# Kernel optimization log

Measured on AMD Instinct MI355X. Metric: run time of the kernel, lower is better.

Reference implementation:

```python
import jax, jax.numpy as jnp
import numpy as np

B, S, C, H, D = 2, 2048, 1024, 16, 64  # hidden C must equal H*D (value is a reshape of key_states)


def setup_inputs() -> dict:
    key = jax.random.key(0)
    ks = jax.random.split(key, 7)
    query_states = jax.random.normal(ks[0], (B, S, C), dtype=jnp.float32)
    key_states = jax.random.normal(ks[1], (B, S, C), dtype=jnp.float32)
    attention_mask = jax.random.randint(ks[2], (B, 1, 1, S), 0, 2).astype(jnp.int32)
    Wq = jax.random.normal(ks[3], (C, H, D), dtype=jnp.float32) * 0.02
    bq = jnp.zeros((H, D), dtype=jnp.float32)
    Wk = jax.random.normal(ks[4], (C, H, D), dtype=jnp.float32) * 0.02
    bk = jnp.zeros((H, D), dtype=jnp.float32)
    return {
        "query_states": query_states,
        "key_states": key_states,
        "attention_mask": attention_mask,
        "Wq": Wq,
        "bq": bq,
        "Wk": Wk,
        "bk": bk,
    }


def reference(query_states, key_states, attention_mask, Wq, bq, Wk, bk):
    # EinsumDense 'abc,cde->abde' with bias on 'de'
    q = jnp.einsum("bsc,chd->bshd", query_states, Wq) + bq  # [B,S,H,D]
    k = jnp.einsum("bsc,chd->bshd", key_states, Wk) + bk    # [B,S,H,D]
    # value is just key_states reshaped into head layout (no projection!)
    v = key_states.reshape(k.shape)                          # [B,S,H,D]
    # scale query by 1/sqrt(dk)
    q = q * jax.lax.rsqrt(jnp.asarray(D, q.dtype))
    # 'aecd,abcd->acbe': a=batch, c=head, b=query pos, e=key pos
    scores = jnp.einsum("bkhd,bqhd->bhqk", k, q)             # [B,H,Sq,Sk]
    mask = (1.0 - attention_mask.astype(scores.dtype)) * -10000.0
    scores = scores + mask
    probs = jax.nn.softmax(scores, axis=-1)
    # dropout is identity at training=False (default)
    # 'acbe,aecd->abcd': weighted sum of values over key positions
    out = jnp.einsum("bhqk,bkhd->bqhd", probs, v)            # [B,S,H,D]
    return out
```

## Files before the change

kernel.cpp:

```cpp
#include <hip/hip_runtime.h>

#define BSZ 2
#define SEQ 2048
#define CH  1024
#define NH  16
#define HD  64
#define LOG2E 1.4426950408889634f

typedef short  bf16x8 __attribute__((ext_vector_type(8)));
typedef short  bf16x4 __attribute__((ext_vector_type(4)));
typedef float  f32x4  __attribute__((ext_vector_type(4)));

__device__ __forceinline__ short f2bf(float f) {
    union { float f; unsigned u; } v; v.f = f;
    unsigned r = v.u + 0x7FFFu + ((v.u >> 16) & 1u);
    return (short)(r >> 16);
}
__device__ __forceinline__ short f2bf_fast(float f) {
    union { float f; unsigned u; } v; v.f = f;
    return (short)((v.u + 0x8000u) >> 16);
}

#if __has_builtin(__builtin_amdgcn_mfma_f32_16x16x16bf16_1k)
__device__ __forceinline__ f32x4 mfma16x16x16(bf16x4 a, bf16x4 b, f32x4 c) {
    return __builtin_amdgcn_mfma_f32_16x16x16bf16_1k(a, b, c, 0, 0, 0);
}
#else
__device__ __forceinline__ f32x4 mfma16x16x16(bf16x4 a, bf16x4 b, f32x4 c) {
    f32x4 d;
    asm("v_mfma_f32_16x16x16_bf16 %0, %1, %2, %3"
        : "=v"(d) : "v"(a), "v"(b), "v"(c));
    return d;
}
#endif

__global__ __launch_bounds__(256) void cast_bf16(
    const float* __restrict__ a, const float* __restrict__ b,
    short* __restrict__ da, short* __restrict__ db)
{
    const float* s = blockIdx.y ? b : a;
    short*       d = blockIdx.y ? db : da;
    long i = ((long)blockIdx.x * 256 + threadIdx.x) * 8;
    float4 v0 = *(const float4*)&s[i];
    float4 v1 = *(const float4*)&s[i + 4];
    bf16x8 o;
    o[0] = f2bf(v0.x); o[1] = f2bf(v0.y); o[2] = f2bf(v0.z); o[3] = f2bf(v0.w);
    o[4] = f2bf(v1.x); o[5] = f2bf(v1.y); o[6] = f2bf(v1.z); o[7] = f2bf(v1.w);
    *(bf16x8*)&d[i] = o;
}

__global__ __launch_bounds__(256) void transpose_cast(
    const float* __restrict__ src, short* __restrict__ dst,
    long sb0, long sb1, long db0, long db1, int srs, int drs)
{
    __shared__ float tile[64][65];
    const int z = blockIdx.z;
    const float* s = src + (long)(z >> 4) * sb0 + (long)(z & 15) * sb1;
    short*       d = dst + (long)(z >> 4) * db0 + (long)(z & 15) * db1;
    const int r0 = blockIdx.y * 64, c0 = blockIdx.x * 64;
    const int tid = threadIdx.x;
    const int r  = tid >> 2;
    const int c4 = (tid & 3) << 4;

    #pragma unroll
    for (int i = 0; i < 16; i += 4) {
        float4 v = *(const float4*)&s[(long)(r0 + r) * srs + c0 + c4 + i];
        tile[r][c4 + i + 0] = v.x;
        tile[r][c4 + i + 1] = v.y;
        tile[r][c4 + i + 2] = v.z;
        tile[r][c4 + i + 3] = v.w;
    }
    __syncthreads();
    bf16x8 o0, o1;
    #pragma unroll
    for (int i = 0; i < 8; i++) o0[i] = f2bf(tile[c4 + i][r]);
    #pragma unroll
    for (int i = 0; i < 8; i++) o1[i] = f2bf(tile[c4 + 8 + i][r]);
    *(bf16x8*)&d[(long)(c0 + r) * drs + r0 + c4 + 0] = o0;
    *(bf16x8*)&d[(long)(c0 + r) * drs + r0 + c4 + 8] = o1;
}

__global__ __launch_bounds__(256) void mask_prep(
    const int* __restrict__ am, float* __restrict__ mf)
{
    int i = blockIdx.x * 256 + threadIdx.x;
    mf[i] = (1.0f - (float)am[i]) * (-10000.0f * LOG2E);
}

__global__ __launch_bounds__(256, 2) void proj_mfma(
    const short* __restrict__ Xq, const short* __restrict__ Xk,
    const short* __restrict__ Wtq, const short* __restrict__ Wtk,
    const float* __restrict__ bq_, const float* __restrict__ bk_,
    short* __restrict__ Yq, short* __restrict__ Yk)
{
    __shared__ short At[128 * 72];
    __shared__ short Bt[128 * 72];
    const int zz = blockIdx.z;
    const short* X    = zz ? Xk  : Xq;
    const short* Wt   = zz ? Wtk : Wtq;
    const float* bias = zz ? bk_ : bq_;
    short*       Y    = zz ? Yk  : Yq;
    const float scale = zz ? 1.0f : (0.125f * LOG2E);

    const int tid  = threadIdx.x;
    const int lane = tid & 63, w = tid >> 6;
    const int quad = lane >> 4, t16 = lane & 15;
    const int m0 = blockIdx.y * 128, n0 = blockIdx.x * 128;
    const int srow = tid >> 1;
    const int shalf = (tid & 1) * 32;

    f32x4 acc[4][4];
    #pragma unroll
    for (int i = 0; i < 4; i++)
        #pragma unroll
        for (int j = 0; j < 4; j++)
            acc[i][j] = (f32x4){0.f, 0.f, 0.f, 0.f};

    const int M0 = (w >> 1) * 64, N0 = (w & 1) * 64;

    bf16x8 ar[4], br[4];
    #pragma unroll
    for (int c = 0; c < 4; c++) {
        ar[c] = *(const bf16x8*)&X [(long)(m0 + srow) * CH + shalf + 8 * c];
        br[c] = *(const bf16x8*)&Wt[(long)(n0 + srow) * CH + shalf + 8 * c];
    }

    for (int k0 = 0; k0 < CH; k0 += 64) {
        __syncthreads();
        #pragma unroll
        for (int c = 0; c < 4; c++) {
            *(bf16x8*)&At[srow * 72 + shalf + 8 * c] = ar[c];
            *(bf16x8*)&Bt[srow * 72 + shalf + 8 * c] = br[c];
        }
        __syncthreads();

        if (k0 + 64 < CH) {
            #pragma unroll
            for (int c = 0; c < 4; c++) {
                ar[c] = *(const bf16x8*)&X [(long)(m0 + srow) * CH + k0 + 64 + shalf + 8 * c];
                br[c] = *(const bf16x8*)&Wt[(long)(n0 + srow) * CH + k0 + 64 + shalf + 8 * c];
            }
        }

        #pragma unroll
        for (int kk = 0; kk < 2; kk++) {
            bf16x8 af[4], bw[4];
            #pragma unroll
            for (int im = 0; im < 4; im++)
                af[im] = *(bf16x8*)&At[(M0 + 16 * im + t16) * 72 + kk * 32 + quad * 8];
            #pragma unroll
            for (int jn = 0; jn < 4; jn++)
                bw[jn] = *(bf16x8*)&Bt[(N0 + 16 * jn + t16) * 72 + kk * 32 + quad * 8];
            #pragma unroll
            for (int im = 0; im < 4; im++)
                #pragma unroll
                for (int jn = 0; jn < 4; jn++)
                    acc[im][jn] = __builtin_amdgcn_mfma_f32_16x16x32_bf16(
                        af[im], bw[jn], acc[im][jn], 0, 0, 0);
        }
    }

    #pragma unroll
    for (int jn = 0; jn < 4; jn++) {
        float bs = bias[n0 + N0 + 16 * jn + t16];
        #pragma unroll
        for (int im = 0; im < 4; im++)
            #pragma unroll
            for (int reg = 0; reg < 4; reg++) {
                float y = (acc[im][jn][reg] + bs) * scale;
                Y[(long)(m0 + M0 + 16 * im + 4 * quad + reg) * (NH * HD)
                  + n0 + N0 + 16 * jn + t16] = f2bf(y);
            }
    }
}

__global__ __launch_bounds__(256, 2) void attn_mfma(
    const short* __restrict__ qp,
    const short* __restrict__ kp,
    const short* __restrict__ vt,
    const float* __restrict__ mf,
    float* __restrict__ out)
{
    __shared__ short Kt[64 * 72];
    __shared__ short Vt[64 * 72];

    const int qt0 = blockIdx.x * 128;
    const int h   = blockIdx.y;
    const int b   = blockIdx.z;
    const int tid = threadIdx.x;
    const int lane = tid & 63, w = tid >> 6;
    const int quad = lane >> 4, t16 = lane & 15;

    bf16x8 qf[2][2];
    #pragma unroll
    for (int qm = 0; qm < 2; qm++)
        #pragma unroll
        for (int ds = 0; ds < 2; ds++)
            qf[qm][ds] = *(const bf16x8*)&qp[
                (long)(b * SEQ + qt0 + w * 32 + qm * 16 + t16) * CH
                + h * HD + ds * 32 + quad * 8];

    f32x4 oa[4][2];
    float l_r[2];
    #pragma unroll
    for (int dt = 0; dt < 4; dt++)
        #pragma unroll
        for (int qm = 0; qm < 2; qm++)
            oa[dt][qm] = (f32x4){0.f, 0.f, 0.f, 0.f};
    l_r[0] = l_r[1] = 0.f;

    const int srow  = tid >> 2;
    const int scol  = (tid & 3) * 16;
    const long kbase = (long)(b * SEQ) * CH + h * HD;
    const long vbase = ((long)(b * NH + h) * HD) * SEQ;

    bf16x8 kr[2], vr[2];
    #pragma unroll
    for (int c = 0; c < 2; c++) {
        kr[c] = *(const bf16x8*)&kp[kbase + (long)srow * CH + scol + 8 * c];
        vr[c] = *(const bf16x8*)&vt[vbase + (long)srow * SEQ + scol + 8 * c];
    }

    for (int kt0 = 0; kt0 < SEQ; kt0 += 64) {
        __syncthreads();
        #pragma unroll
        for (int c = 0; c < 2; c++) {
            *(bf16x8*)&Kt[srow * 72 + scol + 8 * c] = kr[c];
            *(bf16x8*)&Vt[srow * 72 + scol + 8 * c] = vr[c];
        }
        __syncthreads();

        if (kt0 + 64 < SEQ) {
            #pragma unroll
            for (int c = 0; c < 2; c++) {
                kr[c] = *(const bf16x8*)&kp[kbase + (long)(kt0 + 64 + srow) * CH + scol + 8 * c];
                vr[c] = *(const bf16x8*)&vt[vbase + (long)srow * SEQ + kt0 + 64 + scol + 8 * c];
            }
        }

        float4 mv4[4];
        #pragma unroll
        for (int jt = 0; jt < 4; jt++)
            mv4[jt] = *(const float4*)&mf[b * SEQ + kt0 + jt * 16 + quad * 4];

        f32x4 sa[2][4];
        #pragma unroll
        for (int qm = 0; qm < 2; qm++)
            #pragma unroll
            for (int jt = 0; jt < 4; jt++) sa[qm][jt] = (f32x4){0.f, 0.f, 0.f, 0.f};
        #pragma unroll
        for (int ds = 0; ds < 2; ds++) {
            bf16x8 kb[4];
            #pragma unroll
            for (int jt = 0; jt < 4; jt++)
                kb[jt] = *(bf16x8*)&Kt[(jt * 16 + t16) * 72 + ds * 32 + quad * 8];
            #pragma unroll
            for (int qm = 0; qm < 2; qm++)
                #pragma unroll
                for (int jt = 0; jt < 4; jt++)
                    sa[qm][jt] = __builtin_amdgcn_mfma_f32_16x16x32_bf16(
                        kb[jt], qf[qm][ds], sa[qm][jt], 0, 0, 0);
        }

        bf16x4 pb[2][4];
        #pragma unroll
        for (int qm = 0; qm < 2; qm++)
            #pragma unroll
            for (int jt = 0; jt < 4; jt++) {
                float p0 = exp2f(sa[qm][jt][0] + mv4[jt].x);
                float p1 = exp2f(sa[qm][jt][1] + mv4[jt].y);
                float p2 = exp2f(sa[qm][jt][2] + mv4[jt].z);
                float p3 = exp2f(sa[qm][jt][3] + mv4[jt].w);
                l_r[qm] += (p0 + p1) + (p2 + p3);
                bf16x4 pk;
                pk[0] = f2bf_fast(p0); pk[1] = f2bf_fast(p1);
                pk[2] = f2bf_fast(p2); pk[3] = f2bf_fast(p3);
                pb[qm][jt] = pk;
            }

        #pragma unroll
        for (int jt = 0; jt < 4; jt++) {
            bf16x4 va[4];
            #pragma unroll
            for (int dt = 0; dt < 4; dt++)
                va[dt] = *(bf16x4*)&Vt[(dt * 16 + t16) * 72 + jt * 16 + quad * 4];
            #pragma unroll
            for (int dt = 0; dt < 4; dt++)
                #pragma unroll
                for (int qm = 0; qm < 2; qm++)
                    oa[dt][qm] = mfma16x16x16(va[dt], pb[qm][jt], oa[dt][qm]);
        }
    }

    #pragma unroll
    for (int qm = 0; qm < 2; qm++) {
        float l = l_r[qm];
        l += __shfl_xor(l, 16, 64);
        l += __shfl_xor(l, 32, 64);
        float inv = 1.0f / l;
        int q = qt0 + w * 32 + qm * 16 + t16;
        #pragma unroll
        for (int dt = 0; dt < 4; dt++) {
            f32x4 o = oa[dt][qm];
            float4 st = {o[0] * inv, o[1] * inv, o[2] * inv, o[3] * inv};
            *(float4*)&out[((long)(b * SEQ + q) * NH + h) * HD + dt * 16 + quad * 4] = st;
        }
    }
}

extern "C" void kernel_launch(void* const* d_in, const int* in_sizes, int n_in,
                              void* d_out, int out_size, void* d_ws, size_t ws_size,
                              hipStream_t stream) {
    const float* query = (const float*)d_in[0];
    const float* key   = (const float*)d_in[1];
    const int*   amask = (const int*)d_in[2];
    const float* Wq    = (const float*)d_in[3];
    const float* bq    = (const float*)d_in[4];
    const float* Wk    = (const float*)d_in[5];
    const float* bk    = (const float*)d_in[6];
    float* out = (float*)d_out;

    char* ws = (char*)d_ws;
    const long MB = 1024 * 1024;
    short* qc  = (short*)(ws + 0 * MB);
    short* kc  = (short*)(ws + 8 * MB);
    short* qp  = (short*)(ws + 16 * MB);
    short* kp  = (short*)(ws + 24 * MB);
    short* vtr = (short*)(ws + 32 * MB);
    short* wtq = (short*)(ws + 40 * MB);
    short* wtk = (short*)(ws + 42 * MB);
    float* mfv = (float*)(ws + 44 * MB);

    cast_bf16<<<dim3((BSZ * SEQ * CH) / 2048, 2), 256, 0, stream>>>(query, key, qc, kc);

    dim3 wt_grid(16, 16, 1);
    transpose_cast<<<wt_grid, 256, 0, stream>>>(Wq, wtq, 0, 0, 0, 0, CH, CH);
    transpose_cast<<<wt_grid, 256, 0, stream>>>(Wk, wtk, 0, 0, 0, 0, CH, CH);
    dim3 vt_grid(1, SEQ / 64, BSZ * NH);
    transpose_cast<<<vt_grid, 256, 0, stream>>>(
        key, vtr,
        (long)SEQ * CH, (long)HD,
        (long)NH * HD * SEQ, (long)HD * SEQ,
        CH, SEQ);
    mask_prep<<<dim3(BSZ * SEQ / 256), 256, 0, stream>>>(amask, mfv);

    dim3 pgrid((NH * HD) / 128, (BSZ * SEQ) / 128, 2);
    proj_mfma<<<pgrid, 256, 0, stream>>>(qc, kc, wtq, wtk, bq, bk, qp, kp);

    dim3 agrid(SEQ / 128, NH, BSZ);
    attn_mfma<<<agrid, 256, 0, stream>>>(qp, kp, vtr, mfv, out);
}
```

Before: 206.2 us.

## Double-buffer LDS tiles in projection and attention, fold mask into MFMA init

Both the projection GEMM and the attention kernel now use two LDS buffers and a single barrier per iteration. The next tile is written to the alternate buffer while the current one is consumed, and global prefetch runs two tiles ahead. The attention kernel also seeds the score accumulators with the mask bias instead of adding it after the MFMA. It uses the hardware exp2 instruction in place of exp2f, which drops the range handling of the library call. The cost is doubled LDS per block, which may reduce occupancy at two blocks per CU.

```diff
diff --git a/kernel.cpp b/kernel.cpp
--- a/kernel.cpp
+++ b/kernel.cpp
@@ -19,6 +19,15 @@
 __device__ __forceinline__ short f2bf_fast(float f) {
     union { float f; unsigned u; } v; v.f = f;
     return (short)((v.u + 0x8000u) >> 16);
+}
+__device__ __forceinline__ float exp2_hw(float x) {
+#if __has_builtin(__builtin_amdgcn_exp2f)
+    return __builtin_amdgcn_exp2f(x);
+#else
+    float r;
+    asm volatile("v_exp_f32 %0, %1\n\ts_nop 1" : "=v"(r) : "v"(x));
+    return r;
+#endif
 }
 
 #if __has_builtin(__builtin_amdgcn_mfma_f32_16x16x16bf16_1k)
@@ -93,8 +102,8 @@
     const float* __restrict__ bq_, const float* __restrict__ bk_,
     short* __restrict__ Yq, short* __restrict__ Yk)
 {
-    __shared__ short At[128 * 72];
-    __shared__ short Bt[128 * 72];
+    __shared__ short At[2][128 * 72];
+    __shared__ short Bt[2][128 * 72];
     const int zz = blockIdx.z;
     const short* X    = zz ? Xk  : Xq;
     const short* Wt   = zz ? Wtk : Wtq;
@@ -117,6 +126,7 @@
             acc[i][j] = (f32x4){0.f, 0.f, 0.f, 0.f};
 
     const int M0 = (w >> 1) * 64, N0 = (w & 1) * 64;
+    const int NIT = CH / 64;
 
     bf16x8 ar[4], br[4];
     #pragma unroll
@@ -124,21 +134,33 @@
         ar[c] = *(const bf16x8*)&X [(long)(m0 + srow) * CH + shalf + 8 * c];
         br[c] = *(const bf16x8*)&Wt[(long)(n0 + srow) * CH + shalf + 8 * c];
     }
-
-    for (int k0 = 0; k0 < CH; k0 += 64) {
-        __syncthreads();
-        #pragma unroll
-        for (int c = 0; c < 4; c++) {
-            *(bf16x8*)&At[srow * 72 + shalf + 8 * c] = ar[c];
-            *(bf16x8*)&Bt[srow * 72 + shalf + 8 * c] = br[c];
-        }
-        __syncthreads();
-
-        if (k0 + 64 < CH) {
+    #pragma unroll
+    for (int c = 0; c < 4; c++) {
+        *(bf16x8*)&At[0][srow * 72 + shalf + 8 * c] = ar[c];
+        *(bf16x8*)&Bt[0][srow * 72 + shalf + 8 * c] = br[c];
+    }
+    #pragma unroll
+    for (int c = 0; c < 4; c++) {
+        ar[c] = *(const bf16x8*)&X [(long)(m0 + srow) * CH + 64 + shalf + 8 * c];
+        br[c] = *(const bf16x8*)&Wt[(long)(n0 + srow) * CH + 64 + shalf + 8 * c];
+    }
+    __syncthreads();
+
+    for (int it = 0; it < NIT; it++) {
+        const int buf = it & 1;
+        if (it + 1 < NIT) {
             #pragma unroll
             for (int c = 0; c < 4; c++) {
-                ar[c] = *(const bf16x8*)&X [(long)(m0 + srow) * CH + k0 + 64 + shalf + 8 * c];
-                br[c] = *(const bf16x8*)&Wt[(long)(n0 + srow) * CH + k0 + 64 + shalf + 8 * c];
+                *(bf16x8*)&At[buf ^ 1][srow * 72 + shalf + 8 * c] = ar[c];
+                *(bf16x8*)&Bt[buf ^ 1][srow * 72 + shalf + 8 * c] = br[c];
+            }
+            if (it + 2 < NIT) {
+                const long ko = (long)(it + 2) * 64;
+                #pragma unroll
+                for (int c = 0; c < 4; c++) {
+                    ar[c] = *(const bf16x8*)&X [(long)(m0 + srow) * CH + ko + shalf + 8 * c];
+                    br[c] = *(const bf16x8*)&Wt[(long)(n0 + srow) * CH + ko + shalf + 8 * c];
+                }
             }
         }
 
@@ -147,10 +169,10 @@
             bf16x8 af[4], bw[4];
             #pragma unroll
             for (int im = 0; im < 4; im++)
-                af[im] = *(bf16x8*)&At[(M0 + 16 * im + t16) * 72 + kk * 32 + quad * 8];
+                af[im] = *(bf16x8*)&At[buf][(M0 + 16 * im + t16) * 72 + kk * 32 + quad * 8];
             #pragma unroll
             for (int jn = 0; jn < 4; jn++)
-                bw[jn] = *(bf16x8*)&Bt[(N0 + 16 * jn + t16) * 72 + kk * 32 + quad * 8];
+                bw[jn] = *(bf16x8*)&Bt[buf][(N0 + 16 * jn + t16) * 72 + kk * 32 + quad * 8];
             #pragma unroll
             for (int im = 0; im < 4; im++)
                 #pragma unroll
@@ -158,6 +180,7 @@
                     acc[im][jn] = __builtin_amdgcn_mfma_f32_16x16x32_bf16(
                         af[im], bw[jn], acc[im][jn], 0, 0, 0);
         }
+        __syncthreads();
     }
 
     #pragma unroll
@@ -181,8 +204,8 @@
     const float* __restrict__ mf,
     float* __restrict__ out)
 {
-    __shared__ short Kt[64 * 72];
-    __shared__ short Vt[64 * 72];
+    __shared__ short Kt[2][64 * 72];
+    __shared__ short Vt[2][64 * 72];
 
     const int qt0 = blockIdx.x * 128;
     const int h   = blockIdx.y;
@@ -213,6 +236,7 @@
     const int scol  = (tid & 3) * 16;
     const long kbase = (long)(b * SEQ) * CH + h * HD;
     const long vbase = ((long)(b * NH + h) * HD) * SEQ;
+    const int NIT = SEQ / 64;
 
     bf16x8 kr[2], vr[2];
     #pragma unroll
@@ -220,21 +244,35 @@
         kr[c] = *(const bf16x8*)&kp[kbase + (long)srow * CH + scol + 8 * c];
         vr[c] = *(const bf16x8*)&vt[vbase + (long)srow * SEQ + scol + 8 * c];
     }
-
-    for (int kt0 = 0; kt0 < SEQ; kt0 += 64) {
-        __syncthreads();
-        #pragma unroll
-        for (int c = 0; c < 2; c++) {
-            *(bf16x8*)&Kt[srow * 72 + scol + 8 * c] = kr[c];
-            *(bf16x8*)&Vt[srow * 72 + scol + 8 * c] = vr[c];
-        }
-        __syncthreads();
-
-        if (kt0 + 64 < SEQ) {
+    #pragma unroll
+    for (int c = 0; c < 2; c++) {
+        *(bf16x8*)&Kt[0][srow * 72 + scol + 8 * c] = kr[c];
+        *(bf16x8*)&Vt[0][srow * 72 + scol + 8 * c] = vr[c];
+    }
+    #pragma unroll
+    for (int c = 0; c < 2; c++) {
+        kr[c] = *(const bf16x8*)&kp[kbase + (long)(64 + srow) * CH + scol + 8 * c];
+        vr[c] = *(const bf16x8*)&vt[vbase + (long)srow * SEQ + 64 + scol + 8 * c];
+    }
+    __syncthreads();
+
+    for (int it = 0; it < NIT; it++) {
+        const int buf = it & 1;
+        const int kt0 = it * 64;
+
+        if (it + 1 < NIT) {
             #pragma unroll
             for (int c = 0; c < 2; c++) {
-                kr[c] = *(const bf16x8*)&kp[kbase + (long)(kt0 + 64 + srow) * CH + scol + 8 * c];
-                vr[c] = *(const bf16x8*)&vt[vbase + (long)srow * SEQ + kt0 + 64 + scol + 8 * c];
+                *(bf16x8*)&Kt[buf ^ 1][srow * 72 + scol + 8 * c] = kr[c];
+                *(bf16x8*)&Vt[buf ^ 1][srow * 72 + scol + 8 * c] = vr[c];
+            }
+            if (it + 2 < NIT) {
+                const int kn = kt0 + 128;
+                #pragma unroll
+                for (int c = 0; c < 2; c++) {
+                    kr[c] = *(const bf16x8*)&kp[kbase + (long)(kn + srow) * CH + scol + 8 * c];
+                    vr[c] = *(const bf16x8*)&vt[vbase + (long)srow * SEQ + kn + scol + 8 * c];
+                }
             }
         }
 
@@ -247,13 +285,14 @@
         #pragma unroll
         for (int qm = 0; qm < 2; qm++)
             #pragma unroll
-            for (int jt = 0; jt < 4; jt++) sa[qm][jt] = (f32x4){0.f, 0.f, 0.f, 0.f};
+            for (int jt = 0; jt < 4; jt++)
+                sa[qm][jt] = (f32x4){mv4[jt].x, mv4[jt].y, mv4[jt].z, mv4[jt].w};
         #pragma unroll
         for (int ds = 0; ds < 2; ds++) {
             bf16x8 kb[4];
             #pragma unroll
             for (int jt = 0; jt < 4; jt++)
-                kb[jt] = *(bf16x8*)&Kt[(jt * 16 + t16) * 72 + ds * 32 + quad * 8];
+                kb[jt] = *(bf16x8*)&Kt[buf][(jt * 16 + t16) * 72 + ds * 32 + quad * 8];
             #pragma unroll
             for (int qm = 0; qm < 2; qm++)
                 #pragma unroll
@@ -267,10 +306,10 @@
         for (int qm = 0; qm < 2; qm++)
             #pragma unroll
             for (int jt = 0; jt < 4; jt++) {
-                float p0 = exp2f(sa[qm][jt][0] + mv4[jt].x);
-                float p1 = exp2f(sa[qm][jt][1] + mv4[jt].y);
-                float p2 = exp2f(sa[qm][jt][2] + mv4[jt].z);
-                float p3 = exp2f(sa[qm][jt][3] + mv4[jt].w);
+                float p0 = exp2_hw(sa[qm][jt][0]);
+                float p1 = exp2_hw(sa[qm][jt][1]);
+                float p2 = exp2_hw(sa[qm][jt][2]);
+                float p3 = exp2_hw(sa[qm][jt][3]);
                 l_r[qm] += (p0 + p1) + (p2 + p3);
                 bf16x4 pk;
                 pk[0] = f2bf_fast(p0); pk[1] = f2bf_fast(p1);
@@ -283,13 +322,14 @@
             bf16x4 va[4];
             #pragma unroll
             for (int dt = 0; dt < 4; dt++)
-                va[dt] = *(bf16x4*)&Vt[(dt * 16 + t16) * 72 + jt * 16 + quad * 4];
+                va[dt] = *(bf16x4*)&Vt[buf][(dt * 16 + t16) * 72 + jt * 16 + quad * 4];
             #pragma unroll
             for (int dt = 0; dt < 4; dt++)
                 #pragma unroll
                 for (int qm = 0; qm < 2; qm++)
                     oa[dt][qm] = mfma16x16x16(va[dt], pb[qm][jt], oa[dt][qm]);
         }
+        __syncthreads();
     }
 
     #pragma unroll
```

Measured after the change: 181.0 us. 1.14x faster.
